# Kernel optimization log

Measured on AMD Instinct MI355X. Metric: run time of the kernel, lower is better.

## Reference

```python
import jax, jax.numpy as jnp
import numpy as np

B, H, L, D = 2, 8, 512, 64
TEMP = 8.0  # sqrt(D)


def setup_inputs() -> dict:
    key = jax.random.key(0)
    ks = jax.random.split(key, 6)
    q = jax.random.normal(ks[0], (B, H, L, D), jnp.float32)
    k = jax.random.normal(ks[1], (B, H, L, D), jnp.float32)
    v = jax.random.normal(ks[2], (B, H, L, D), jnp.float32)
    adj_k = jax.random.normal(ks[3], (B, L, L, D), jnp.float32)
    adj_v = jax.random.normal(ks[4], (B, L, L, D), jnp.float32)
    mask = jax.random.randint(ks[5], (B, 1, 1, L), 0, 2, jnp.int32)
    return {"q": q, "k": k, "v": v, "adj_k": adj_k, "adj_v": adj_v, "mask": mask}


def reference(q, k, v, adj_k, adj_v, mask):
    qs = q / TEMP
    # standard QK^T term + relation term: score[b,h,i,j] += q[b,h,i]. adj_k[b,i,j]
    attn = jnp.einsum('bhid,bhjd->bhij', qs, k) + jnp.einsum('bhid,bijd->bhij', qs, adj_k)
    attn = jnp.where(mask == 0, jnp.float32(-10000.0), attn)
    attn = jax.nn.softmax(attn, axis=-1)  # dropout p=0 (eval / deterministic)
    # standard AV term + relation term: out[b,h,i] += sum_j attn[b,h,i,j]*adj_v[b,i,j]
    out = jnp.einsum('bhij,bhjd->bhid', attn, v) + jnp.einsum('bhij,bijd->bhid', attn, adj_v)
    return out, attn
```

## Files before the change

kernel.cpp:

```cpp
#include <hip/hip_runtime.h>

constexpr int B  = 2;
constexpr int NH = 8;
constexpr int L  = 512;
constexpr int D  = 64;
constexpr float INV_TEMP = 0.125f;

__global__ __launch_bounds__(256) void k1_qk(const float* __restrict__ q,
                                             const float* __restrict__ k,
                                             float* __restrict__ s1) {
  const int bh = blockIdx.x, it = blockIdx.y, jt = blockIdx.z;
  __shared__ float As[64][65];
  __shared__ float Bs[64][65];
  const int t = threadIdx.x;
  const float* qb = q + ((size_t)bh * L + it * 64) * D;
  const float* kb = k + ((size_t)bh * L + jt * 64) * D;
#pragma unroll
  for (int n = 0; n < 4; ++n) {
    int idx = t + (n << 8);
    int r = idx >> 4, c = (idx & 15) << 2;
    float4 a = *(const float4*)(qb + r * D + c);
    As[r][c] = a.x * INV_TEMP; As[r][c + 1] = a.y * INV_TEMP;
    As[r][c + 2] = a.z * INV_TEMP; As[r][c + 3] = a.w * INV_TEMP;
    float4 bb = *(const float4*)(kb + r * D + c);
    Bs[r][c] = bb.x; Bs[r][c + 1] = bb.y; Bs[r][c + 2] = bb.z; Bs[r][c + 3] = bb.w;
  }
  __syncthreads();
  const int ti = (t >> 4) << 2, tj = (t & 15) << 2;
  float acc[4][4] = {};
#pragma unroll 8
  for (int kk = 0; kk < 64; ++kk) {
    float a0 = As[ti][kk], a1 = As[ti + 1][kk], a2 = As[ti + 2][kk], a3 = As[ti + 3][kk];
    float b0 = Bs[tj][kk], b1 = Bs[tj + 1][kk], b2 = Bs[tj + 2][kk], b3 = Bs[tj + 3][kk];
    acc[0][0] += a0 * b0; acc[0][1] += a0 * b1; acc[0][2] += a0 * b2; acc[0][3] += a0 * b3;
    acc[1][0] += a1 * b0; acc[1][1] += a1 * b1; acc[1][2] += a1 * b2; acc[1][3] += a1 * b3;
    acc[2][0] += a2 * b0; acc[2][1] += a2 * b1; acc[2][2] += a2 * b2; acc[2][3] += a2 * b3;
    acc[3][0] += a3 * b0; acc[3][1] += a3 * b1; acc[3][2] += a3 * b2; acc[3][3] += a3 * b3;
  }
  float* srow = s1 + ((size_t)bh * L + it * 64) * L + jt * 64;
#pragma unroll
  for (int m = 0; m < 4; ++m)
    *(float4*)(srow + (size_t)(it * 0 + ti + m) * L + tj) =
        make_float4(acc[m][0], acc[m][1], acc[m][2], acc[m][3]);
}

__global__ __launch_bounds__(256) void k2_rel_softmax(const float* __restrict__ q,
                                                      const float* __restrict__ adj_k,
                                                      const int* __restrict__ mask,
                                                      float* __restrict__ attn) {
  const int b = blockIdx.x >> 9, i = blockIdx.x & (L - 1);
  __shared__ float qs[NH][D];
  __shared__ float sc[NH][L];
  __shared__ float ak[64][65];
  const int t = threadIdx.x;
  for (int n = t; n < NH * D; n += 256) {
    int h = n >> 6, d = n & 63;
    qs[h][d] = q[(((size_t)b * NH + h) * L + i) * D + d] * INV_TEMP;
  }
  const float* akb = adj_k + ((size_t)b * L + i) * (size_t)L * D;
  const int j = t & 63, hq = t >> 6;
  for (int jt = 0; jt < L; jt += 64) {
    __syncthreads();
#pragma unroll
    for (int n = 0; n < 4; ++n) {
      int idx = t + (n << 8);
      int r = idx >> 4, c = (idx & 15) << 2;
      float4 a = *(const float4*)(akb + (size_t)(jt + r) * D + c);
      ak[r][c] = a.x; ak[r][c + 1] = a.y; ak[r][c + 2] = a.z; ak[r][c + 3] = a.w;
    }
    __syncthreads();
    float acc0 = 0.f, acc1 = 0.f;
#pragma unroll
    for (int d = 0; d < 64; d += 4) {
      float4 q0 = *(const float4*)&qs[hq][d];
      float4 q1 = *(const float4*)&qs[hq + 4][d];
      float k0 = ak[j][d], k1 = ak[j][d + 1], k2 = ak[j][d + 2], k3 = ak[j][d + 3];
      acc0 += q0.x * k0 + q0.y * k1 + q0.z * k2 + q0.w * k3;
      acc1 += q1.x * k0 + q1.y * k1 + q1.z * k2 + q1.w * k3;
    }
    sc[hq][jt + j] = acc0;
    sc[hq + 4][jt + j] = acc1;
  }
  __syncthreads();
  const int h = t >> 5, l = t & 31;
  float* s1row = attn + (((size_t)b * NH + h) * L + i) * L;
  const int* mrow = mask + b * L;
  float vals[16];
  float mx = -3.4e38f;
#pragma unroll
  for (int m = 0; m < 16; ++m) {
    int jj = l + (m << 5);
    float vsc = sc[h][jj] + s1row[jj];
    vsc = (mrow[jj] == 0) ? -10000.0f : vsc;
    vals[m] = vsc;
    mx = fmaxf(mx, vsc);
  }
#pragma unroll
  for (int off = 16; off > 0; off >>= 1) mx = fmaxf(mx, __shfl_xor(mx, off, 32));
  float sum = 0.f;
#pragma unroll
  for (int m = 0; m < 16; ++m) { vals[m] = __expf(vals[m] - mx); sum += vals[m]; }
#pragma unroll
  for (int off = 16; off > 0; off >>= 1) sum += __shfl_xor(sum, off, 32);
  const float inv = 1.0f / sum;
#pragma unroll
  for (int m = 0; m < 16; ++m) s1row[l + (m << 5)] = vals[m] * inv;
}

__global__ __launch_bounds__(256) void k3a_av(const float* __restrict__ attn,
                                              const float* __restrict__ v,
                                              float* __restrict__ out) {
  const int bh = blockIdx.x, it = blockIdx.y;
  __shared__ float At[64][65];
  __shared__ float Vt[64][65];
  const int t = threadIdx.x;
  const float* arow = attn + ((size_t)bh * L + it * 64) * L;
  const float* vb = v + (size_t)bh * L * D;
  const int ti = (t >> 4) << 2, td = (t & 15) << 2;
  float acc[4][4] = {};
  for (int jt = 0; jt < L; jt += 64) {
    __syncthreads();
#pragma unroll
    for (int n = 0; n < 4; ++n) {
      int idx = t + (n << 8);
      int r = idx >> 4, c = (idx & 15) << 2;
      float4 a = *(const float4*)(arow + (size_t)r * L + jt + c);
      At[r][c] = a.x; At[r][c + 1] = a.y; At[r][c + 2] = a.z; At[r][c + 3] = a.w;
      float4 vv = *(const float4*)(vb + (size_t)(jt + r) * D + c);
      Vt[r][c] = vv.x; Vt[r][c + 1] = vv.y; Vt[r][c + 2] = vv.z; Vt[r][c + 3] = vv.w;
    }
    __syncthreads();
#pragma unroll 8
    for (int jj = 0; jj < 64; ++jj) {
      float a0 = At[ti][jj], a1 = At[ti + 1][jj], a2 = At[ti + 2][jj], a3 = At[ti + 3][jj];
      float b0 = Vt[jj][td], b1 = Vt[jj][td + 1], b2 = Vt[jj][td + 2], b3 = Vt[jj][td + 3];
      acc[0][0] += a0 * b0; acc[0][1] += a0 * b1; acc[0][2] += a0 * b2; acc[0][3] += a0 * b3;
      acc[1][0] += a1 * b0; acc[1][1] += a1 * b1; acc[1][2] += a1 * b2; acc[1][3] += a1 * b3;
      acc[2][0] += a2 * b0; acc[2][1] += a2 * b1; acc[2][2] += a2 * b2; acc[2][3] += a2 * b3;
      acc[3][0] += a3 * b0; acc[3][1] += a3 * b1; acc[3][2] += a3 * b2; acc[3][3] += a3 * b3;
    }
  }
  float* orow = out + ((size_t)bh * L + it * 64) * D;
#pragma unroll
  for (int m = 0; m < 4; ++m)
    *(float4*)(orow + (size_t)(ti + m) * D + td) =
        make_float4(acc[m][0], acc[m][1], acc[m][2], acc[m][3]);
}

__global__ __launch_bounds__(256) void k3b_rel_out(const float* __restrict__ attn,
                                                   const float* __restrict__ adj_v,
                                                   float* __restrict__ out) {
  const int b = blockIdx.x >> 9, i = blockIdx.x & (L - 1);
  __shared__ float at[NH][L];
  __shared__ float av[64][65];
  const int t = threadIdx.x;
  float* atf = &at[0][0];
  for (int n = t; n < NH * L; n += 256) {
    int h = n >> 9, jj = n & (L - 1);
    atf[n] = attn[(((size_t)b * NH + h) * L + i) * L + jj];
  }
  const float* avb = adj_v + ((size_t)b * L + i) * (size_t)L * D;
  const int d = t & 63, h0 = t >> 6;
  float acc0 = 0.f, acc1 = 0.f;
  for (int jt = 0; jt < L; jt += 64) {
    __syncthreads();
#pragma unroll
    for (int n = 0; n < 4; ++n) {
      int idx = t + (n << 8);
      int r = idx >> 4, c = (idx & 15) << 2;
      float4 a = *(const float4*)(avb + (size_t)(jt + r) * D + c);
      av[r][c] = a.x; av[r][c + 1] = a.y; av[r][c + 2] = a.z; av[r][c + 3] = a.w;
    }
    __syncthreads();
#pragma unroll
    for (int jj = 0; jj < 64; jj += 4) {
      float4 a0 = *(const float4*)&at[h0][jt + jj];
      float4 a1 = *(const float4*)&at[h0 + 4][jt + jj];
      float v0 = av[jj][d], v1 = av[jj + 1][d], v2 = av[jj + 2][d], v3 = av[jj + 3][d];
      acc0 += a0.x * v0 + a0.y * v1 + a0.z * v2 + a0.w * v3;
      acc1 += a1.x * v0 + a1.y * v1 + a1.z * v2 + a1.w * v3;
    }
  }
  const size_t o0 = (((size_t)b * NH + h0) * L + i) * D + d;
  out[o0] += acc0;
  out[o0 + (size_t)4 * L * D] += acc1;
}

extern "C" void kernel_launch(void* const* d_in, const int* in_sizes, int n_in,
                              void* d_out, int out_size, void* d_ws, size_t ws_size,
                              hipStream_t stream) {
  const float* q     = (const float*)d_in[0];
  const float* k     = (const float*)d_in[1];
  const float* v     = (const float*)d_in[2];
  const float* adj_k = (const float*)d_in[3];
  const float* adj_v = (const float*)d_in[4];
  const int*   mask  = (const int*)d_in[5];
  float* out  = (float*)d_out;
  float* attn = out + (size_t)B * NH * L * D;

  dim3 g1(B * NH, L / 64, L / 64);
  k1_qk<<<g1, 256, 0, stream>>>(q, k, attn);
  k2_rel_softmax<<<B * L, 256, 0, stream>>>(q, adj_k, mask, attn);
  dim3 g3(B * NH, L / 64);
  k3a_av<<<g3, 256, 0, stream>>>(attn, v, out);
  k3b_rel_out<<<B * L, 256, 0, stream>>>(attn, adj_v, out);
}
```

Measured before the change: 354.0 us.

## Fuse QK, relation scores, softmax and AV into one per-row kernel

Replaces the four kernels with a single kernel per (batch, query row). It computes q·(k+adj_k) directly, runs the softmax, keeps the probabilities in shared memory and computes attn·(v+adj_v) without re-reading attn from global memory. This removes the intermediate score round trips, the attn re-read and three launches. In exchange, k and v are now streamed from global/L2 once per query row instead of being reused through shared-memory GEMM tiles, which adds a lot of redundant traffic.

New measurement: 491.3 us. +38.8%, slower.

```diff
diff --git a/kernel.cpp b/kernel.cpp
--- a/kernel.cpp
+++ b/kernel.cpp
@@ -6,184 +6,116 @@
 constexpr int D  = 64;
 constexpr float INV_TEMP = 0.125f;
 
-__global__ __launch_bounds__(256) void k1_qk(const float* __restrict__ q,
-                                             const float* __restrict__ k,
-                                             float* __restrict__ s1) {
-  const int bh = blockIdx.x, it = blockIdx.y, jt = blockIdx.z;
-  __shared__ float As[64][65];
-  __shared__ float Bs[64][65];
+__global__ __launch_bounds__(256, 4) void fused_attn(
+    const float* __restrict__ q, const float* __restrict__ k,
+    const float* __restrict__ v, const float* __restrict__ adj_k,
+    const float* __restrict__ adj_v, const int* __restrict__ mask,
+    float* __restrict__ out, float* __restrict__ attn) {
+  const int b = blockIdx.x >> 9, i = blockIdx.x & (L - 1);
   const int t = threadIdx.x;
-  const float* qb = q + ((size_t)bh * L + it * 64) * D;
-  const float* kb = k + ((size_t)bh * L + jt * 64) * D;
-#pragma unroll
-  for (int n = 0; n < 4; ++n) {
-    int idx = t + (n << 8);
-    int r = idx >> 4, c = (idx & 15) << 2;
-    float4 a = *(const float4*)(qb + r * D + c);
-    As[r][c] = a.x * INV_TEMP; As[r][c + 1] = a.y * INV_TEMP;
-    As[r][c + 2] = a.z * INV_TEMP; As[r][c + 3] = a.w * INV_TEMP;
-    float4 bb = *(const float4*)(kb + r * D + c);
-    Bs[r][c] = bb.x; Bs[r][c + 1] = bb.y; Bs[r][c + 2] = bb.z; Bs[r][c + 3] = bb.w;
-  }
-  __syncthreads();
-  const int ti = (t >> 4) << 2, tj = (t & 15) << 2;
-  float acc[4][4] = {};
-#pragma unroll 8
-  for (int kk = 0; kk < 64; ++kk) {
-    float a0 = As[ti][kk], a1 = As[ti + 1][kk], a2 = As[ti + 2][kk], a3 = As[ti + 3][kk];
-    float b0 = Bs[tj][kk], b1 = Bs[tj + 1][kk], b2 = Bs[tj + 2][kk], b3 = Bs[tj + 3][kk];
-    acc[0][0] += a0 * b0; acc[0][1] += a0 * b1; acc[0][2] += a0 * b2; acc[0][3] += a0 * b3;
-    acc[1][0] += a1 * b0; acc[1][1] += a1 * b1; acc[1][2] += a1 * b2; acc[1][3] += a1 * b3;
-    acc[2][0] += a2 * b0; acc[2][1] += a2 * b1; acc[2][2] += a2 * b2; acc[2][3] += a2 * b3;
-    acc[3][0] += a3 * b0; acc[3][1] += a3 * b1; acc[3][2] += a3 * b2; acc[3][3] += a3 * b3;
-  }
-  float* srow = s1 + ((size_t)bh * L + it * 64) * L + jt * 64;
-#pragma unroll
-  for (int m = 0; m < 4; ++m)
-    *(float4*)(srow + (size_t)(it * 0 + ti + m) * L + tj) =
-        make_float4(acc[m][0], acc[m][1], acc[m][2], acc[m][3]);
-}
-
-__global__ __launch_bounds__(256) void k2_rel_softmax(const float* __restrict__ q,
-                                                      const float* __restrict__ adj_k,
-                                                      const int* __restrict__ mask,
-                                                      float* __restrict__ attn) {
-  const int b = blockIdx.x >> 9, i = blockIdx.x & (L - 1);
   __shared__ float qs[NH][D];
   __shared__ float sc[NH][L];
-  __shared__ float ak[64][65];
-  const int t = threadIdx.x;
+
   for (int n = t; n < NH * D; n += 256) {
     int h = n >> 6, d = n & 63;
     qs[h][d] = q[(((size_t)b * NH + h) * L + i) * D + d] * INV_TEMP;
   }
+  __syncthreads();
+
   const float* akb = adj_k + ((size_t)b * L + i) * (size_t)L * D;
-  const int j = t & 63, hq = t >> 6;
-  for (int jt = 0; jt < L; jt += 64) {
-    __syncthreads();
+  const float* kb  = k + (size_t)b * NH * L * D;
+  const int j1 = t, j2 = t + 256;
+  float acc1[NH] = {}, acc2[NH] = {};
 #pragma unroll
-    for (int n = 0; n < 4; ++n) {
-      int idx = t + (n << 8);
-      int r = idx >> 4, c = (idx & 15) << 2;
-      float4 a = *(const float4*)(akb + (size_t)(jt + r) * D + c);
-      ak[r][c] = a.x; ak[r][c + 1] = a.y; ak[r][c + 2] = a.z; ak[r][c + 3] = a.w;
+  for (int dc = 0; dc < D; dc += 16) {
+    float4 a1[4], a2[4];
+#pragma unroll
+    for (int u = 0; u < 4; ++u) {
+      a1[u] = *(const float4*)(akb + (size_t)j1 * D + dc + 4 * u);
+      a2[u] = *(const float4*)(akb + (size_t)j2 * D + dc + 4 * u);
     }
-    __syncthreads();
-    float acc0 = 0.f, acc1 = 0.f;
 #pragma unroll
-    for (int d = 0; d < 64; d += 4) {
-      float4 q0 = *(const float4*)&qs[hq][d];
-      float4 q1 = *(const float4*)&qs[hq + 4][d];
-      float k0 = ak[j][d], k1 = ak[j][d + 1], k2 = ak[j][d + 2], k3 = ak[j][d + 3];
-      acc0 += q0.x * k0 + q0.y * k1 + q0.z * k2 + q0.w * k3;
-      acc1 += q1.x * k0 + q1.y * k1 + q1.z * k2 + q1.w * k3;
+    for (int h = 0; h < NH; ++h) {
+      const float* k1p = kb + ((size_t)h * L + j1) * D + dc;
+      const float* k2p = kb + ((size_t)h * L + j2) * D + dc;
+      float s1 = acc1[h], s2 = acc2[h];
+#pragma unroll
+      for (int u = 0; u < 4; ++u) {
+        float4 qv = *(const float4*)&qs[h][dc + 4 * u];
+        float4 k1 = *(const float4*)(k1p + 4 * u);
+        float4 k2 = *(const float4*)(k2p + 4 * u);
+        s1 = fmaf(qv.x, a1[u].x + k1.x, s1);
+        s1 = fmaf(qv.y, a1[u].y + k1.y, s1);
+        s1 = fmaf(qv.z, a1[u].z + k1.z, s1);
+        s1 = fmaf(qv.w, a1[u].w + k1.w, s1);
+        s2 = fmaf(qv.x, a2[u].x + k2.x, s2);
+        s2 = fmaf(qv.y, a2[u].y + k2.y, s2);
+        s2 = fmaf(qv.z, a2[u].z + k2.z, s2);
+        s2 = fmaf(qv.w, a2[u].w + k2.w, s2);
+      }
+      acc1[h] = s1; acc2[h] = s2;
     }
-    sc[hq][jt + j] = acc0;
-    sc[hq + 4][jt + j] = acc1;
+  }
+#pragma unroll
+  for (int h = 0; h < NH; ++h) {
+    sc[h][j1] = acc1[h];
+    sc[h][j2] = acc2[h];
   }
   __syncthreads();
-  const int h = t >> 5, l = t & 31;
-  float* s1row = attn + (((size_t)b * NH + h) * L + i) * L;
-  const int* mrow = mask + b * L;
-  float vals[16];
-  float mx = -3.4e38f;
+
+  {
+    const int h = t >> 5, l = t & 31;
+    const int* mrow = mask + b * L;
+    float* arow = attn + (((size_t)b * NH + h) * L + i) * L;
+    float vals[16];
+    float mx = -3.4e38f;
 #pragma unroll
-  for (int m = 0; m < 16; ++m) {
-    int jj = l + (m << 5);
-    float vsc = sc[h][jj] + s1row[jj];
-    vsc = (mrow[jj] == 0) ? -10000.0f : vsc;
-    vals[m] = vsc;
-    mx = fmaxf(mx, vsc);
-  }
+    for (int m = 0; m < 16; ++m) {
+      int jj = l + (m << 5);
+      float vsc = sc[h][jj];
+      vsc = (mrow[jj] == 0) ? -10000.0f : vsc;
+      vals[m] = vsc;
+      mx = fmaxf(mx, vsc);
+    }
 #pragma unroll
-  for (int off = 16; off > 0; off >>= 1) mx = fmaxf(mx, __shfl_xor(mx, off, 32));
-  float sum = 0.f;
+    for (int off = 16; off > 0; off >>= 1) mx = fmaxf(mx, __shfl_xor(mx, off, 32));
+    float sum = 0.f;
 #pragma unroll
-  for (int m = 0; m < 16; ++m) { vals[m] = __expf(vals[m] - mx); sum += vals[m]; }
+    for (int m = 0; m < 16; ++m) { vals[m] = __expf(vals[m] - mx); sum += vals[m]; }
 #pragma unroll
-  for (int off = 16; off > 0; off >>= 1) sum += __shfl_xor(sum, off, 32);
-  const float inv = 1.0f / sum;
+    for (int off = 16; off > 0; off >>= 1) sum += __shfl_xor(sum, off, 32);
+    const float inv = 1.0f / sum;
 #pragma unroll
-  for (int m = 0; m < 16; ++m) s1row[l + (m << 5)] = vals[m] * inv;
-}
-
-__global__ __launch_bounds__(256) void k3a_av(const float* __restrict__ attn,
-                                              const float* __restrict__ v,
-                                              float* __restrict__ out) {
-  const int bh = blockIdx.x, it = blockIdx.y;
-  __shared__ float At[64][65];
-  __shared__ float Vt[64][65];
-  const int t = threadIdx.x;
-  const float* arow = attn + ((size_t)bh * L + it * 64) * L;
-  const float* vb = v + (size_t)bh * L * D;
-  const int ti = (t >> 4) << 2, td = (t & 15) << 2;
-  float acc[4][4] = {};
-  for (int jt = 0; jt < L; jt += 64) {
-    __syncthreads();
-#pragma unroll
-    for (int n = 0; n < 4; ++n) {
-      int idx = t + (n << 8);
-      int r = idx >> 4, c = (idx & 15) << 2;
-      float4 a = *(const float4*)(arow + (size_t)r * L + jt + c);
-      At[r][c] = a.x; At[r][c + 1] = a.y; At[r][c + 2] = a.z; At[r][c + 3] = a.w;
-      float4 vv = *(const float4*)(vb + (size_t)(jt + r) * D + c);
-      Vt[r][c] = vv.x; Vt[r][c + 1] = vv.y; Vt[r][c + 2] = vv.z; Vt[r][c + 3] = vv.w;
-    }
-    __syncthreads();
-#pragma unroll 8
-    for (int jj = 0; jj < 64; ++jj) {
-      float a0 = At[ti][jj], a1 = At[ti + 1][jj], a2 = At[ti + 2][jj], a3 = At[ti + 3][jj];
-      float b0 = Vt[jj][td], b1 = Vt[jj][td + 1], b2 = Vt[jj][td + 2], b3 = Vt[jj][td + 3];
-      acc[0][0] += a0 * b0; acc[0][1] += a0 * b1; acc[0][2] += a0 * b2; acc[0][3] += a0 * b3;
-      acc[1][0] += a1 * b0; acc[1][1] += a1 * b1; acc[1][2] += a1 * b2; acc[1][3] += a1 * b3;
-      acc[2][0] += a2 * b0; acc[2][1] += a2 * b1; acc[2][2] += a2 * b2; acc[2][3] += a2 * b3;
-      acc[3][0] += a3 * b0; acc[3][1] += a3 * b1; acc[3][2] += a3 * b2; acc[3][3] += a3 * b3;
+    for (int m = 0; m < 16; ++m) {
+      int jj = l + (m << 5);
+      float p = vals[m] * inv;
+      arow[jj] = p;
+      sc[h][jj] = p;
     }
   }
-  float* orow = out + ((size_t)bh * L + it * 64) * D;
-#pragma unroll
-  for (int m = 0; m < 4; ++m)
-    *(float4*)(orow + (size_t)(ti + m) * D + td) =
-        make_float4(acc[m][0], acc[m][1], acc[m][2], acc[m][3]);
-}
+  __syncthreads();
 
-__global__ __launch_bounds__(256) void k3b_rel_out(const float* __restrict__ attn,
-                                                   const float* __restrict__ adj_v,
-                                                   float* __restrict__ out) {
-  const int b = blockIdx.x >> 9, i = blockIdx.x & (L - 1);
-  __shared__ float at[NH][L];
-  __shared__ float av[64][65];
-  const int t = threadIdx.x;
-  float* atf = &at[0][0];
-  for (int n = t; n < NH * L; n += 256) {
-    int h = n >> 9, jj = n & (L - 1);
-    atf[n] = attn[(((size_t)b * NH + h) * L + i) * L + jj];
+  {
+    const int d = t & 63, h0 = t >> 6;
+    const float* avb = adj_v + ((size_t)b * L + i) * (size_t)L * D + d;
+    const float* vp0 = v + (((size_t)b * NH + h0) * L) * D + d;
+    const float* vp1 = v + (((size_t)b * NH + h0 + 4) * L) * D + d;
+    float o0a = 0.f, o0b = 0.f, o1a = 0.f, o1b = 0.f;
+#pragma unroll 2
+    for (int j = 0; j < L; j += 2) {
+      float av0 = avb[(size_t)j * D];
+      float av1 = avb[(size_t)(j + 1) * D];
+      float p00 = sc[h0][j],     p01 = sc[h0][j + 1];
+      float p10 = sc[h0 + 4][j], p11 = sc[h0 + 4][j + 1];
+      o0a = fmaf(p00, av0 + vp0[(size_t)j * D], o0a);
+      o0b = fmaf(p01, av1 + vp0[(size_t)(j + 1) * D], o0b);
+      o1a = fmaf(p10, av0 + vp1[(size_t)j * D], o1a);
+      o1b = fmaf(p11, av1 + vp1[(size_t)(j + 1) * D], o1b);
+    }
+    const size_t ob = (((size_t)b * NH + h0) * L + i) * D + d;
+    out[ob] = o0a + o0b;
+    out[ob + (size_t)4 * L * D] = o1a + o1b;
   }
-  const float* avb = adj_v + ((size_t)b * L + i) * (size_t)L * D;
-  const int d = t & 63, h0 = t >> 6;
-  float acc0 = 0.f, acc1 = 0.f;
-  for (int jt = 0; jt < L; jt += 64) {
-    __syncthreads();
-#pragma unroll
-    for (int n = 0; n < 4; ++n) {
-      int idx = t + (n << 8);
-      int r = idx >> 4, c = (idx & 15) << 2;
-      float4 a = *(const float4*)(avb + (size_t)(jt + r) * D + c);
-      av[r][c] = a.x; av[r][c + 1] = a.y; av[r][c + 2] = a.z; av[r][c + 3] = a.w;
-    }
-    __syncthreads();
-#pragma unroll
-    for (int jj = 0; jj < 64; jj += 4) {
-      float4 a0 = *(const float4*)&at[h0][jt + jj];
-      float4 a1 = *(const float4*)&at[h0 + 4][jt + jj];
-      float v0 = av[jj][d], v1 = av[jj + 1][d], v2 = av[jj + 2][d], v3 = av[jj + 3][d];
-      acc0 += a0.x * v0 + a0.y * v1 + a0.z * v2 + a0.w * v3;
-      acc1 += a1.x * v0 + a1.y * v1 + a1.z * v2 + a1.w * v3;
-    }
-  }
-  const size_t o0 = (((size_t)b * NH + h0) * L + i) * D + d;
-  out[o0] += acc0;
-  out[o0 + (size_t)4 * L * D] += acc1;
 }
 
 extern "C" void kernel_launch(void* const* d_in, const int* in_sizes, int n_in,
@@ -198,10 +130,5 @@
   float* out  = (float*)d_out;
   float* attn = out + (size_t)B * NH * L * D;
 
-  dim3 g1(B * NH, L / 64, L / 64);
-  k1_qk<<<g1, 256, 0, stream>>>(q, k, attn);
-  k2_rel_softmax<<<B * L, 256, 0, stream>>>(q, adj_k, mask, attn);
-  dim3 g3(B * NH, L / 64);
-  k3a_av<<<g3, 256, 0, stream>>>(attn, v, out);
-  k3b_rel_out<<<B * L, 256, 0, stream>>>(attn, adj_v, out);
+  fused_attn<<<B * L, 256, 0, stream>>>(q, k, v, adj_k, adj_v, mask, out, attn);
 }
```
